# Optimization experiments

Hardware: AMD Instinct MI355X
Metric: run time of the kernel (lower is better)

## Reference

```python
import jax, jax.numpy as jnp
import numpy as np

B, D, HIST = 32768, 128, 30     # batch, d_model, history length
M, H, RANK = 15, 4, 8           # memory_length, d_hidden, operator max_rank


def spectral_op(W, sigma_scale, sigma_shift, alpha, residual_scale):
    """W' = alpha * (U diag(f(S)) Vh) + residual_scale * W, f(S)=softplus(scale)*S+shift.
    W: (h, d) 2D matrix (h=4 < RANK so k = h and no tail singular values remain)."""
    U, S, Vh = jnp.linalg.svd(W, full_matrices=False)   # U:(h,h) S:(h,) Vh:(h,d)
    k = min(RANK, S.shape[-1])
    scale = jax.nn.softplus(sigma_scale[:k])
    S_new = scale * S[:k] + sigma_shift[:k]
    if S.shape[-1] > k:
        S_new = jnp.concatenate([S_new, S[k:]], axis=-1)
    W_spec = (U * S_new[None, :]) @ Vh
    return alpha * W_spec + residual_scale * W


def setup_inputs() -> dict:
    key = jax.random.key(0)
    k0, k1 = jax.random.split(key)
    return {
        "pre_acts_history": jax.random.normal(k0, (B, D, HIST), jnp.float32),
        "weights_1": jax.random.normal(k1, (M, H, D), jnp.float32) * 0.02,
        "bias_1": jnp.zeros((1, H, D), jnp.float32),
        "bias_2": jnp.zeros((1, H, D), jnp.float32),
        "bias_3": jnp.zeros((1, D), jnp.float32),
        "contract_weights": jnp.ones((M,), jnp.float32) / M,
        "sigma_scale": jnp.ones((RANK,), jnp.float32),
        "sigma_shift": jnp.zeros((RANK,), jnp.float32),
        "alpha": jnp.full((1,), 0.7, jnp.float32),          # 1 - residual_blend
        "residual_scale": jnp.full((1,), 0.3, jnp.float32),  # residual_blend
    }


def reference(pre_acts_history, weights_1, bias_1, bias_2, bias_3,
              contract_weights, sigma_scale, sigma_shift, alpha, residual_scale):
    a = alpha[0]
    r = residual_scale[0]
    inputs = pre_acts_history[..., -M:]                         # (B, D, M)
    # layer 1: per-d contraction over memory
    h1 = jnp.einsum('bdM,Mhd->bdh', inputs, weights_1)
    h1 = jax.nn.relu(h1 + jnp.transpose(bias_1, (0, 2, 1)))     # (B, D, H)
    # derive W2 = T(contract(W1)), W3 = T(W2)
    w = jax.nn.softmax(contract_weights)
    W1_c = jnp.einsum('m,mhd->hd', w, weights_1)                # (H, D)
    W2 = spectral_op(W1_c, sigma_scale, sigma_shift, a, r)      # (H, D)
    # layer 2: elementwise gating ('bdh,hd->bdh')
    h2 = jax.nn.relu(h1 * W2.T[None] + jnp.transpose(bias_2, (0, 2, 1)))
    W3 = spectral_op(W2, sigma_scale, sigma_shift, a, r)        # (H, D)
    out = jnp.einsum('bdh,hd->bd', h2, W3) + bias_3             # (B, D)
    return out
```

## Files before the change

kernel.cpp:

```cpp
#include <hip/hip_runtime.h>
#include <math.h>

#define B_N    32768
#define D_N    128
#define HIST_N 30
#define M_N    15
#define H_N    4

#define TILE_ROWS   256
#define TILE_FLOATS (TILE_ROWS * HIST_N)
#define TILE_BYTES  (TILE_FLOATS * 4)
#define WAVE_FLOATS (TILE_FLOATS / 4)
#define WAVE_BYTES  (WAVE_FLOATS * 4)
#define NBLOCKS     512
#define TPB         (B_N * D_N / TILE_ROWS / NBLOCKS)
#define LOADS_PER_TILE 9

__device__ __forceinline__ void gload16(const void* g, float* l) {
    __builtin_amdgcn_global_load_lds(
        (const __attribute__((address_space(1))) unsigned int*)g,
        (__attribute__((address_space(3))) unsigned int*)l, 16, 0, 0);
}
__device__ __forceinline__ void gload4(const void* g, float* l) {
    __builtin_amdgcn_global_load_lds(
        (const __attribute__((address_space(1))) unsigned int*)g,
        (__attribute__((address_space(3))) unsigned int*)l, 4, 0, 0);
}

__global__ __launch_bounds__(256, 2) void fused_kernel(
        const float* __restrict__ pa,
        const float* __restrict__ w1,
        const float* __restrict__ b1,
        const float* __restrict__ b2,
        const float* __restrict__ b3,
        const float* __restrict__ cw,
        const float* __restrict__ ss,
        const float* __restrict__ sh,
        const float* __restrict__ al,
        const float* __restrict__ rs,
        float* __restrict__ out) {
    const int tid   = threadIdx.x;
    const int lane  = tid & 63;
    const int wv_id = tid >> 6;
    const int d     = tid & 127;

    __shared__ __align__(16) float lds[2][TILE_FLOATS];
    __shared__ float W1c[H_N][D_N];
    __shared__ float Gsh[16];
    __shared__ float Msh[32];

    const char* pab = (const char*)pa;
    const size_t tile0 = (size_t)blockIdx.x * TPB;

    auto issue_tile = [&](size_t t, int buf) {
        const char* gw = pab + t * TILE_BYTES + (size_t)wv_id * WAVE_BYTES;
        float* lw = &lds[buf][0] + wv_id * WAVE_FLOATS;
#pragma unroll
        for (int c = 0; c < 7; ++c)
            gload16(gw + c * 1024 + lane * 16, lw + c * 256);
#pragma unroll
        for (int c = 0; c < 2; ++c)
            gload4(gw + 7168 + c * 256 + lane * 4, lw + 1792 + c * 64);
    };

    issue_tile(tile0, 0);
    issue_tile(tile0 + 1, 1);

    float wv[M_N][H_N];
#pragma unroll
    for (int m = 0; m < M_N; ++m)
#pragma unroll
        for (int h = 0; h < H_N; ++h)
            wv[m][h] = w1[(m * H_N + h) * D_N + d];

    float b1v[H_N], b2v[H_N];
#pragma unroll
    for (int h = 0; h < H_N; ++h) {
        b1v[h] = b1[h * D_N + d];
        b2v[h] = b2[h * D_N + d];
    }
    const float b3v = b3[d];

    float swm[M_N];
    {
        float mx = cw[0];
#pragma unroll
        for (int m = 1; m < M_N; ++m) mx = fmaxf(mx, cw[m]);
        float s = 0.f;
#pragma unroll
        for (int m = 0; m < M_N; ++m) { swm[m] = expf(cw[m] - mx); s += swm[m]; }
        float inv = 1.f / s;
#pragma unroll
        for (int m = 0; m < M_N; ++m) swm[m] *= inv;
    }

    if (tid < 128) {
#pragma unroll
        for (int h = 0; h < H_N; ++h) {
            float acc = 0.f;
#pragma unroll
            for (int m = 0; m < M_N; ++m) acc = fmaf(swm[m], wv[m][h], acc);
            W1c[h][tid] = acc;
        }
    }
    asm volatile("s_waitcnt lgkmcnt(0)" ::: "memory");
    __builtin_amdgcn_s_barrier();

    if (tid < 16) {
        const int i = tid >> 2, j = tid & 3;
        float s = 0.f;
        for (int st = 0; st < 128; ++st) {
            int dd = (st + tid * 8) & 127;
            s = fmaf(W1c[i][dd], W1c[j][dd], s);
        }
        Gsh[tid] = s;
    }
    asm volatile("s_waitcnt lgkmcnt(0)" ::: "memory");
    __builtin_amdgcn_s_barrier();

    if (tid == 0) {
        float G[4][4], U[4][4];
#pragma unroll
        for (int i = 0; i < 4; ++i)
#pragma unroll
            for (int j = 0; j < 4; ++j) {
                G[i][j] = Gsh[i * 4 + j];
                U[i][j] = (i == j) ? 1.f : 0.f;
            }
        for (int sweep = 0; sweep < 6; ++sweep)
            for (int p = 0; p < 3; ++p)
                for (int q = p + 1; q < 4; ++q) {
                    float apq = G[p][q];
                    if (fabsf(apq) < 1e-30f) continue;
                    float theta = (G[q][q] - G[p][p]) / (2.f * apq);
                    float t = ((theta >= 0.f) ? 1.f : -1.f) /
                              (fabsf(theta) + sqrtf(theta * theta + 1.f));
                    float c = 1.f / sqrtf(t * t + 1.f), sn = t * c;
                    for (int i = 0; i < 4; ++i) {
                        float gip = G[i][p], giq = G[i][q];
                        G[i][p] = c * gip - sn * giq;
                        G[i][q] = sn * gip + c * giq;
                    }
                    for (int i = 0; i < 4; ++i) {
                        float gpi = G[p][i], gqi = G[q][i];
                        G[p][i] = c * gpi - sn * gqi;
                        G[q][i] = sn * gpi + c * gqi;
                    }
                    for (int i = 0; i < 4; ++i) {
                        float uip = U[i][p], uiq = U[i][q];
                        U[i][p] = c * uip - sn * uiq;
                        U[i][q] = sn * uip + c * uiq;
                    }
                }
        float lam[4];
#pragma unroll
        for (int i = 0; i < 4; ++i) lam[i] = G[i][i];
        int ord[4] = {0, 1, 2, 3};
        for (int i = 0; i < 4; ++i)
            for (int j = i + 1; j < 4; ++j)
                if (lam[ord[j]] > lam[ord[i]]) { int t2 = ord[i]; ord[i] = ord[j]; ord[j] = t2; }

        const float a = al[0], r = rs[0];
        float c1[4], S2a[4];
        for (int p = 0; p < 4; ++p) {
            int e = ord[p];
            float S = sqrtf(fmaxf(lam[e], 0.f));
            float x = ss[p];
            float sp = (x > 20.f) ? x : log1pf(expf(x));
            float ratio = (S > 1e-30f) ? ((sp * S + sh[p]) / S) : sp;
            c1[e] = a * ratio + r;
            S2a[e] = fabsf(c1[e]) * S;
        }
        int ord2[4] = {0, 1, 2, 3};
        for (int i = 0; i < 4; ++i)
            for (int j = i + 1; j < 4; ++j)
                if (S2a[ord2[j]] > S2a[ord2[i]]) { int t2 = ord2[i]; ord2[i] = ord2[j]; ord2[j] = t2; }
        float c12[4];
        for (int p = 0; p < 4; ++p) {
            int e = ord2[p];
            float Sa = S2a[e];
            float x = ss[p];
            float sp = (x > 20.f) ? x : log1pf(expf(x));
            float ratio2 = (Sa > 1e-30f) ? ((sp * Sa + sh[p]) / Sa) : sp;
            c12[e] = (a * ratio2 + r) * c1[e];
        }
#pragma unroll
        for (int i = 0; i < 4; ++i)
#pragma unroll
            for (int j = 0; j < 4; ++j) {
                float m2 = 0.f, m3 = 0.f;
#pragma unroll
                for (int e = 0; e < 4; ++e) {
                    float uu = U[i][e] * U[j][e];
                    m2 = fmaf(uu, c1[e], m2);
                    m3 = fmaf(uu, c12[e], m3);
                }
                Msh[i * 4 + j] = m2;
                Msh[16 + i * 4 + j] = m3;
            }
    }
    asm volatile("s_waitcnt lgkmcnt(0)" ::: "memory");
    __builtin_amdgcn_s_barrier();

    float w2v[H_N], w3v[H_N];
#pragma unroll
    for (int h = 0; h < H_N; ++h) {
        float s2 = 0.f, s3 = 0.f;
#pragma unroll
        for (int k4 = 0; k4 < 4; ++k4) {
            float wc = W1c[k4][d];
            s2 = fmaf(Msh[h * 4 + k4], wc, s2);
            s3 = fmaf(Msh[16 + h * 4 + k4], wc, s3);
        }
        w2v[h] = s2;
        w3v[h] = s3;
    }

#pragma unroll 2
    for (int k = 0; k < TPB; ++k) {
        if (k == TPB - 1)
            asm volatile("s_waitcnt vmcnt(0)" ::: "memory");
        else
            asm volatile("s_waitcnt vmcnt(9)" ::: "memory");

        const float* L = &lds[k & 1][0] + tid * HIST_N + (HIST_N - M_N);
        float x0 = L[0];
        float h1[H_N];
#pragma unroll
        for (int h = 0; h < H_N; ++h) h1[h] = x0 * wv[0][h];
#pragma unroll
        for (int c = 0; c < 7; ++c) {
            float2 q = *(const float2*)(L + 1 + 2 * c);
#pragma unroll
            for (int h = 0; h < H_N; ++h) h1[h] = fmaf(q.x, wv[1 + 2 * c][h], h1[h]);
#pragma unroll
            for (int h = 0; h < H_N; ++h) h1[h] = fmaf(q.y, wv[2 + 2 * c][h], h1[h]);
        }
        float acc = b3v;
#pragma unroll
        for (int h = 0; h < H_N; ++h) {
            float v = fmaxf(h1[h] + b1v[h], 0.f);
            float u = fmaxf(fmaf(v, w2v[h], b2v[h]), 0.f);
            acc = fmaf(u, w3v[h], acc);
        }
        out[(tile0 + k) * TILE_ROWS + tid] = acc;

        asm volatile("" ::: "memory");
        if (k + 2 < TPB) issue_tile(tile0 + k + 2, k & 1);
    }
}

extern "C" void kernel_launch(void* const* d_in, const int* in_sizes, int n_in,
                              void* d_out, int out_size, void* d_ws, size_t ws_size,
                              hipStream_t stream) {
    const float* pa = (const float*)d_in[0];
    const float* w1 = (const float*)d_in[1];
    const float* b1 = (const float*)d_in[2];
    const float* b2 = (const float*)d_in[3];
    const float* b3 = (const float*)d_in[4];
    const float* cw = (const float*)d_in[5];
    const float* ss = (const float*)d_in[6];
    const float* sh = (const float*)d_in[7];
    const float* al = (const float*)d_in[8];
    const float* rs = (const float*)d_in[9];
    float* out = (float*)d_out;

    fused_kernel<<<NBLOCKS, 256, 0, stream>>>(pa, w1, b1, b2, b3, cw, ss, sh, al, rs, out);
}
```

Before: 121.7 us.

## Stage only the last 16 history floats per row into LDS with 16-byte loads

Instead of copying every full 30-float row into LDS, each wave now issues four 16-byte global-to-LDS loads per row group that fetch only floats 14..29, the part that holds the 15 used memory steps. This shrinks LDS per tile and the count of load instructions, and reads each row with float4 LDS loads. Block count is doubled and the occupancy hint is raised to 3 blocks per CU. DRAM traffic may change little because 64-byte segments inside 120-byte rows still touch most cache lines, and the rows are now read with strided rather than contiguous access.

```diff
diff --git a/kernel.cpp b/kernel.cpp
--- a/kernel.cpp
+++ b/kernel.cpp
@@ -8,26 +8,22 @@
 #define H_N    4
 
 #define TILE_ROWS   256
-#define TILE_FLOATS (TILE_ROWS * HIST_N)
-#define TILE_BYTES  (TILE_FLOATS * 4)
-#define WAVE_FLOATS (TILE_FLOATS / 4)
-#define WAVE_BYTES  (WAVE_FLOATS * 4)
-#define NBLOCKS     512
+#define ROW_BYTES   (HIST_N * 4)
+#define TILE_BYTES  (TILE_ROWS * ROW_BYTES)
+#define STG_ROW_F   16
+#define STG_TILE_F  (TILE_ROWS * STG_ROW_F)
+#define WAVE_ROWS   64
+#define NBLOCKS     1024
 #define TPB         (B_N * D_N / TILE_ROWS / NBLOCKS)
-#define LOADS_PER_TILE 9
+#define LOADS_PER_TILE 4
 
 __device__ __forceinline__ void gload16(const void* g, float* l) {
     __builtin_amdgcn_global_load_lds(
         (const __attribute__((address_space(1))) unsigned int*)g,
         (__attribute__((address_space(3))) unsigned int*)l, 16, 0, 0);
 }
-__device__ __forceinline__ void gload4(const void* g, float* l) {
-    __builtin_amdgcn_global_load_lds(
-        (const __attribute__((address_space(1))) unsigned int*)g,
-        (__attribute__((address_space(3))) unsigned int*)l, 4, 0, 0);
-}
-
-__global__ __launch_bounds__(256, 2) void fused_kernel(
+
+__global__ __launch_bounds__(256, 3) void fused_kernel(
         const float* __restrict__ pa,
         const float* __restrict__ w1,
         const float* __restrict__ b1,
@@ -42,9 +38,10 @@
     const int tid   = threadIdx.x;
     const int lane  = tid & 63;
     const int wv_id = tid >> 6;
-    const int d     = tid & 127;
-
-    __shared__ __align__(16) float lds[2][TILE_FLOATS];
+    const int row_w = lane;
+    const int d     = (wv_id * WAVE_ROWS + row_w) & (D_N - 1);
+
+    __shared__ __align__(16) float lds[2][STG_TILE_F];
     __shared__ float W1c[H_N][D_N];
     __shared__ float Gsh[16];
     __shared__ float Msh[32];
@@ -53,14 +50,12 @@
     const size_t tile0 = (size_t)blockIdx.x * TPB;
 
     auto issue_tile = [&](size_t t, int buf) {
-        const char* gw = pab + t * TILE_BYTES + (size_t)wv_id * WAVE_BYTES;
-        float* lw = &lds[buf][0] + wv_id * WAVE_FLOATS;
-#pragma unroll
-        for (int c = 0; c < 7; ++c)
-            gload16(gw + c * 1024 + lane * 16, lw + c * 256);
-#pragma unroll
-        for (int c = 0; c < 2; ++c)
-            gload4(gw + 7168 + c * 256 + lane * 4, lw + 1792 + c * 64);
+        const char* gw = pab + t * TILE_BYTES + (size_t)wv_id * WAVE_ROWS * ROW_BYTES
+                         + (size_t)(lane & 15) * ROW_BYTES + 56 + (lane >> 4) * 16;
+        float* lw = &lds[buf][0] + wv_id * (WAVE_ROWS * STG_ROW_F);
+#pragma unroll
+        for (int g = 0; g < 4; ++g)
+            gload16(gw + g * (16 * ROW_BYTES), lw + g * 256);
     };
 
     issue_tile(tile0, 0);
@@ -99,7 +94,8 @@
         for (int h = 0; h < H_N; ++h) {
             float acc = 0.f;
 #pragma unroll
-            for (int m = 0; m < M_N; ++m) acc = fmaf(swm[m], wv[m][h], acc);
+            for (int m = 0; m < M_N; ++m)
+                acc = fmaf(swm[m], w1[(m * H_N + h) * D_N + tid], acc);
             W1c[h][tid] = acc;
         }
     }
@@ -216,26 +212,32 @@
         w3v[h] = s3;
     }
 
-#pragma unroll 2
+    const int rd_base = wv_id * (WAVE_ROWS * STG_ROW_F)
+                      + (row_w >> 4) * 256 + (row_w & 15) * 4;
+
     for (int k = 0; k < TPB; ++k) {
         if (k == TPB - 1)
             asm volatile("s_waitcnt vmcnt(0)" ::: "memory");
         else
-            asm volatile("s_waitcnt vmcnt(9)" ::: "memory");
-
-        const float* L = &lds[k & 1][0] + tid * HIST_N + (HIST_N - M_N);
-        float x0 = L[0];
-        float h1[H_N];
-#pragma unroll
-        for (int h = 0; h < H_N; ++h) h1[h] = x0 * wv[0][h];
-#pragma unroll
-        for (int c = 0; c < 7; ++c) {
-            float2 q = *(const float2*)(L + 1 + 2 * c);
-#pragma unroll
-            for (int h = 0; h < H_N; ++h) h1[h] = fmaf(q.x, wv[1 + 2 * c][h], h1[h]);
-#pragma unroll
-            for (int h = 0; h < H_N; ++h) h1[h] = fmaf(q.y, wv[2 + 2 * c][h], h1[h]);
-        }
+            asm volatile("s_waitcnt vmcnt(4)" ::: "memory");
+
+        const float* L = &lds[k & 1][0] + rd_base;
+        float4 x4[4];
+#pragma unroll
+        for (int c = 0; c < 4; ++c)
+            x4[c] = *(const float4*)(L + c * 64);
+
+        const float xe[16] = {x4[0].x, x4[0].y, x4[0].z, x4[0].w,
+                              x4[1].x, x4[1].y, x4[1].z, x4[1].w,
+                              x4[2].x, x4[2].y, x4[2].z, x4[2].w,
+                              x4[3].x, x4[3].y, x4[3].z, x4[3].w};
+        float h1[H_N] = {0.f, 0.f, 0.f, 0.f};
+#pragma unroll
+        for (int m = 0; m < M_N; ++m)
+#pragma unroll
+            for (int h = 0; h < H_N; ++h)
+                h1[h] = fmaf(xe[1 + m], wv[m][h], h1[h]);
+
         float acc = b3v;
 #pragma unroll
         for (int h = 0; h < H_N; ++h) {
@@ -243,7 +245,7 @@
             float u = fmaxf(fmaf(v, w2v[h], b2v[h]), 0.f);
             acc = fmaf(u, w3v[h], acc);
         }
-        out[(tile0 + k) * TILE_ROWS + tid] = acc;
+        out[(tile0 + k) * TILE_ROWS + wv_id * WAVE_ROWS + row_w] = acc;
 
         asm volatile("" ::: "memory");
         if (k + 2 < TPB) issue_tile(tile0 + k + 2, k & 1);
```

Measured after the change: 155.6 us. 1.28x slower.

## Stage input tiles through registers instead of direct global-to-LDS loads

Applied to the files above, without the earlier changes.

Replaces the asynchronous global_load_lds tile streaming with vectorised float4 loads into registers, followed by explicit LDS writes. The loads are double-buffered in two register sets so the next tile's global read overlaps the current tile's compute. A workgroup barrier is added per tile, because each wave no longer loads only the rows it consumes. The W1c reduction now rereads weights from global memory rather than keeping them live in registers. The trade-off is higher register use and per-tile synchronisation, in exchange for wider loads.

```diff
diff --git a/kernel.cpp b/kernel.cpp
--- a/kernel.cpp
+++ b/kernel.cpp
@@ -9,23 +9,9 @@
 
 #define TILE_ROWS   256
 #define TILE_FLOATS (TILE_ROWS * HIST_N)
-#define TILE_BYTES  (TILE_FLOATS * 4)
-#define WAVE_FLOATS (TILE_FLOATS / 4)
-#define WAVE_BYTES  (WAVE_FLOATS * 4)
+#define TILE_F4     (TILE_FLOATS / 4)
 #define NBLOCKS     512
 #define TPB         (B_N * D_N / TILE_ROWS / NBLOCKS)
-#define LOADS_PER_TILE 9
-
-__device__ __forceinline__ void gload16(const void* g, float* l) {
-    __builtin_amdgcn_global_load_lds(
-        (const __attribute__((address_space(1))) unsigned int*)g,
-        (__attribute__((address_space(3))) unsigned int*)l, 16, 0, 0);
-}
-__device__ __forceinline__ void gload4(const void* g, float* l) {
-    __builtin_amdgcn_global_load_lds(
-        (const __attribute__((address_space(1))) unsigned int*)g,
-        (__attribute__((address_space(3))) unsigned int*)l, 4, 0, 0);
-}
 
 __global__ __launch_bounds__(256, 2) void fused_kernel(
         const float* __restrict__ pa,
@@ -44,27 +30,29 @@
     const int wv_id = tid >> 6;
     const int d     = tid & 127;
 
-    __shared__ __align__(16) float lds[2][TILE_FLOATS];
+    __shared__ __align__(16) float4 lds4[2][TILE_F4];
     __shared__ float W1c[H_N][D_N];
     __shared__ float Gsh[16];
     __shared__ float Msh[32];
 
-    const char* pab = (const char*)pa;
+    const float4* pa4 = (const float4*)pa;
     const size_t tile0 = (size_t)blockIdx.x * TPB;
 
-    auto issue_tile = [&](size_t t, int buf) {
-        const char* gw = pab + t * TILE_BYTES + (size_t)wv_id * WAVE_BYTES;
-        float* lw = &lds[buf][0] + wv_id * WAVE_FLOATS;
-#pragma unroll
-        for (int c = 0; c < 7; ++c)
-            gload16(gw + c * 1024 + lane * 16, lw + c * 256);
-#pragma unroll
-        for (int c = 0; c < 2; ++c)
-            gload4(gw + 7168 + c * 256 + lane * 4, lw + 1792 + c * 64);
+    auto load_tile = [&](size_t t, float4* r) {
+        const float4* src = pa4 + t * TILE_F4;
+#pragma unroll
+        for (int j = 0; j < 7; ++j) r[j] = src[j * 256 + tid];
+        if (lane < 32) r[7] = src[1792 + wv_id * 32 + lane];
     };
-
-    issue_tile(tile0, 0);
-    issue_tile(tile0 + 1, 1);
+    auto write_tile = [&](int buf, const float4* r) {
+        float4* L4 = &lds4[buf][0];
+#pragma unroll
+        for (int j = 0; j < 7; ++j) L4[j * 256 + tid] = r[j];
+        if (lane < 32) L4[1792 + wv_id * 32 + lane] = r[7];
+    };
+
+    float4 rA[8], rB[8];
+    load_tile(tile0, rA);
 
     float wv[M_N][H_N];
 #pragma unroll
@@ -99,7 +87,8 @@
         for (int h = 0; h < H_N; ++h) {
             float acc = 0.f;
 #pragma unroll
-            for (int m = 0; m < M_N; ++m) acc = fmaf(swm[m], wv[m][h], acc);
+            for (int m = 0; m < M_N; ++m)
+                acc = fmaf(swm[m], w1[(m * H_N + h) * D_N + tid], acc);
             W1c[h][tid] = acc;
         }
     }
@@ -216,14 +205,8 @@
         w3v[h] = s3;
     }
 
-#pragma unroll 2
-    for (int k = 0; k < TPB; ++k) {
-        if (k == TPB - 1)
-            asm volatile("s_waitcnt vmcnt(0)" ::: "memory");
-        else
-            asm volatile("s_waitcnt vmcnt(9)" ::: "memory");
-
-        const float* L = &lds[k & 1][0] + tid * HIST_N + (HIST_N - M_N);
+    auto compute_tile = [&](int buf, size_t t) {
+        const float* L = (const float*)&lds4[buf][0] + tid * HIST_N + (HIST_N - M_N);
         float x0 = L[0];
         float h1[H_N];
 #pragma unroll
@@ -243,10 +226,25 @@
             float u = fmaxf(fmaf(v, w2v[h], b2v[h]), 0.f);
             acc = fmaf(u, w3v[h], acc);
         }
-        out[(tile0 + k) * TILE_ROWS + tid] = acc;
-
-        asm volatile("" ::: "memory");
-        if (k + 2 < TPB) issue_tile(tile0 + k + 2, k & 1);
+        out[t * TILE_ROWS + tid] = acc;
+    };
+
+    for (int k = 0; k < TPB; k += 2) {
+        if (k + 1 < TPB) load_tile(tile0 + k + 1, rB);
+        write_tile(k & 1 ? 1 : 0, rA);
+        asm volatile("s_waitcnt lgkmcnt(0)" ::: "memory");
+        __builtin_amdgcn_s_barrier();
+        asm volatile("" ::: "memory");
+        compute_tile(0, tile0 + k);
+        asm volatile("" ::: "memory");
+
+        if (k + 2 < TPB) load_tile(tile0 + k + 2, rA);
+        write_tile(1, rB);
+        asm volatile("s_waitcnt lgkmcnt(0)" ::: "memory");
+        __builtin_amdgcn_s_barrier();
+        asm volatile("" ::: "memory");
+        compute_tile(1, tile0 + k + 1);
+        asm volatile("" ::: "memory");
     }
 }
 
```

Measured after the change: 253.5 us. +108.3%, slower.
